# Optimization experiments

Hardware: AMD Instinct MI355X
Metric: run time of the kernel (lower is better)

Reference implementation:

```python
import jax, jax.numpy as jnp
import numpy as np

B, C, H, W = 4, 256, 64, 64
DQ = C // 8

def setup_inputs() -> dict:
    key = jax.random.key(0)
    ks = jax.random.split(key, 7)
    x = jax.random.normal(ks[0], (B, C, H, W), dtype=jnp.float32)
    # 1x1 convs == per-pixel linear layers: weight [out, in], bias [out]
    Wq = jax.random.normal(ks[1], (DQ, C), dtype=jnp.float32) * (1.0 / np.sqrt(C))
    bq = jax.random.normal(ks[2], (DQ,), dtype=jnp.float32) * 0.01
    Wk = jax.random.normal(ks[3], (DQ, C), dtype=jnp.float32) * (1.0 / np.sqrt(C))
    bk = jax.random.normal(ks[4], (DQ,), dtype=jnp.float32) * 0.01
    Wv = jax.random.normal(ks[5], (C, C), dtype=jnp.float32) * (1.0 / np.sqrt(C))
    bv = jax.random.normal(ks[6], (C,), dtype=jnp.float32) * 0.01
    return {"x": x, "Wq": Wq, "bq": bq, "Wk": Wk, "bk": bk, "Wv": Wv, "bv": bv}

def reference(x, Wq, bq, Wk, bk, Wv, bv):
    b, c, h, w = x.shape
    n = h * w
    xf = x.reshape(b, c, n)                                  # [b,c,n]
    Q = jnp.einsum('dc,bcn->bnd', Wq, xf) + bq               # [b,n,dq]
    K = jnp.einsum('dc,bcn->bdn', Wk, xf) + bk[None, :, None]  # [b,dq,n]
    A = jax.nn.softmax(jnp.einsum('bnd,bdm->bnm', Q, K), axis=-1)  # [b,n,n]
    V = jnp.einsum('oc,bcn->bon', Wv, xf) + bv[None, :, None]      # [b,c,n]
    # torch: bmm(V, A^T) -> out[b,c,i] = sum_j V[b,c,j] * A[b,i,j]
    out = jnp.einsum('bcj,bij->bci', V, A)
    return x + out.reshape(b, c, h, w)
```

## Files before the change

kernel.cpp:

```cpp
#include <hip/hip_runtime.h>
#include <math.h>

#define BB 4
#define CC 256
#define NN 4096
#define DQ 32
#define LOG2E 1.44269504f

typedef _Float16 half8 __attribute__((ext_vector_type(8)));
typedef _Float16 half4 __attribute__((ext_vector_type(4)));
typedef float float4v __attribute__((ext_vector_type(4)));

__global__ __launch_bounds__(64) void prep_kernel(
    const float* __restrict__ Wq, const float* __restrict__ bq,
    const float* __restrict__ Wk, const float* __restrict__ bk,
    const float* __restrict__ Wv, const float* __restrict__ bv,
    _Float16* __restrict__ Wh, float* __restrict__ bh)
{
    int o = blockIdx.x, t = threadIdx.x;
    const float* src; float scale = 1.0f, bias;
    if (o < DQ)            { src = Wq + o * CC;        scale = LOG2E; bias = bq[o] * LOG2E; }
    else if (o < 2 * DQ)   { src = Wk + (o - DQ) * CC;                bias = bk[o - DQ]; }
    else                   { src = Wv + (o - 2 * DQ) * CC;            bias = bv[o - 2 * DQ]; }
    float4 v = *(const float4*)(src + t * 4);
    half4 h = { (_Float16)(v.x * scale), (_Float16)(v.y * scale),
                (_Float16)(v.z * scale), (_Float16)(v.w * scale) };
    *(half4*)(Wh + o * CC + t * 4) = h;
    if (t == 0) bh[o] = bias;
}

__global__ __launch_bounds__(256) void proj_kernel(
    const float* __restrict__ x, const _Float16* __restrict__ Wh,
    const float* __restrict__ bh,
    _Float16* __restrict__ Qt, _Float16* __restrict__ Kt,
    _Float16* __restrict__ Vh)
{
    __shared__ _Float16 xl[32 * 256];
    __shared__ _Float16 os_qk[32 * 72];
    __shared__ _Float16 os_v[256 * 40];

    const int tid = threadIdx.x;
    const int lane = tid & 63, w = tid >> 6;
    const int i16 = lane & 15, q = lane >> 4;
    const int n0 = blockIdx.x * 32, b = blockIdx.y;

    const float* xb = x + (size_t)b * CC * NN + n0;
    #pragma unroll
    for (int u = 0; u < 8; ++u) {
        int idx = u * 256 + tid;
        int c = idx >> 3, n4 = idx & 7;
        float4 v = *(const float4*)(xb + (size_t)c * NN + n4 * 4);
        int chunk = c >> 3, cl = c & 7;
        float vv[4] = {v.x, v.y, v.z, v.w};
        #pragma unroll
        for (int e = 0; e < 4; ++e) {
            int n = n4 * 4 + e;
            xl[n * 256 + ((chunk ^ n) * 8) + cl] = (_Float16)vv[e];
        }
    }

    float4v acc[5][2];
    const int obase = 80 * w;
    #pragma unroll
    for (int ot = 0; ot < 5; ++ot) {
        float4 b4 = *(const float4*)(bh + obase + 16 * ot + 4 * q);
        #pragma unroll
        for (int nt = 0; nt < 2; ++nt)
            acc[ot][nt] = (float4v){b4.x, b4.y, b4.z, b4.w};
    }
    __syncthreads();

    #pragma unroll
    for (int k = 0; k < 8; ++k) {
        half8 af[5], bf[2];
        #pragma unroll
        for (int ot = 0; ot < 5; ++ot)
            af[ot] = *(const half8*)(Wh + (size_t)(obase + 16 * ot + i16) * CC + k * 32 + 8 * q);
        #pragma unroll
        for (int nt = 0; nt < 2; ++nt) {
            int n = 16 * nt + i16;
            bf[nt] = *(const half8*)&xl[n * 256 + (((4 * k + q) ^ n) * 8)];
        }
        #pragma unroll
        for (int ot = 0; ot < 5; ++ot)
            #pragma unroll
            for (int nt = 0; nt < 2; ++nt)
                acc[ot][nt] = __builtin_amdgcn_mfma_f32_16x16x32_f16(af[ot], bf[nt], acc[ot][nt], 0, 0, 0);
    }

    #pragma unroll
    for (int ot = 0; ot < 5; ++ot) {
        int og = obase + 16 * ot;
        #pragma unroll
        for (int nt = 0; nt < 2; ++nt) {
            int n = 16 * nt + i16;
            if (og < 64) {
                half4 hv = { (_Float16)acc[ot][nt][0], (_Float16)acc[ot][nt][1],
                             (_Float16)acc[ot][nt][2], (_Float16)acc[ot][nt][3] };
                *(half4*)&os_qk[n * 72 + og + 4 * q] = hv;
            } else {
                int cb = og - 64 + 4 * q;
                #pragma unroll
                for (int r = 0; r < 4; ++r)
                    os_v[(cb + r) * 40 + n] = (_Float16)acc[ot][nt][r];
            }
        }
    }
    __syncthreads();

    _Float16* Qtb = Qt + (size_t)b * NN * DQ;
    _Float16* Ktb = Kt + (size_t)b * NN * DQ;
    {
        int n = tid >> 3, p = tid & 7;
        half8 hv = *(const half8*)&os_qk[n * 72 + 8 * p];
        if (p < 4) *(half8*)(Qtb + (size_t)(n0 + n) * DQ + 8 * p) = hv;
        else       *(half8*)(Ktb + (size_t)(n0 + n) * DQ + 8 * (p - 4)) = hv;
    }
    _Float16* Vb = Vh + (size_t)b * CC * NN;
    #pragma unroll
    for (int u = 0; u < 4; ++u) {
        int c = u * 64 + (tid >> 2), p = tid & 3;
        half8 hv = *(const half8*)&os_v[c * 40 + 8 * p];
        *(half8*)(Vb + (size_t)c * NN + n0 + 8 * p) = hv;
    }
}

__global__ __launch_bounds__(256) void attn_kernel(
    const float* __restrict__ x,
    const _Float16* __restrict__ Qt, const _Float16* __restrict__ Kt,
    const _Float16* __restrict__ Vh,
    float* __restrict__ out)
{
    __shared__ _Float16 k2[2][16 * 64];
    __shared__ _Float16 v2[3][64 * 64];
    __shared__ _Float16 ps[2][32 * 40];
    __shared__ float    stx[4][32];

    const int tid = threadIdx.x;
    const int w = tid >> 6, lane = tid & 63;
    const int i16 = lane & 15, q = lane >> 4;
    const int i0 = blockIdx.x * 32, cs = blockIdx.y, b = blockIdx.z;
    const int c0 = cs * 128;

    const _Float16* Ktb = Kt + (size_t)b * NN * DQ;
    const _Float16* Vb  = Vh + (size_t)b * CC * NN + (size_t)c0 * NN;

    half8 qb[2];
    {
        const _Float16* Qtb = Qt + (size_t)b * NN * DQ;
        qb[0] = *(const half8*)(Qtb + (size_t)(i0 + i16) * DQ + 8 * q);
        qb[1] = *(const half8*)(Qtb + (size_t)(i0 + 16 + i16) * DQ + 8 * q);
    }

    float mA[2] = {-INFINITY, -INFINITY};
    {
        const _Float16* kq = Ktb + (size_t)(1024 * w) * DQ;
        half8 kf[4];
        #pragma unroll
        for (int u = 0; u < 4; ++u)
            kf[u] = *(const half8*)(kq + (size_t)(16 * u + i16) * DQ + 8 * q);
        for (int t = 0; t < 64; t += 4) {
            #pragma unroll
            for (int u = 0; u < 4; ++u) {
                half8 ka = kf[u];
                int nt = t + 4 + u;
                if (nt < 64)
                    kf[u] = *(const half8*)(kq + (size_t)(16 * nt + i16) * DQ + 8 * q);
                float4v z = {0.f, 0.f, 0.f, 0.f};
                float4v s0 = __builtin_amdgcn_mfma_f32_16x16x32_f16(ka, qb[0], z, 0, 0, 0);
                float4v s1 = __builtin_amdgcn_mfma_f32_16x16x32_f16(ka, qb[1], z, 0, 0, 0);
                mA[0] = fmaxf(mA[0], fmaxf(fmaxf(s0[0], s0[1]), fmaxf(s0[2], s0[3])));
                mA[1] = fmaxf(mA[1], fmaxf(fmaxf(s1[0], s1[1]), fmaxf(s1[2], s1[3])));
            }
        }
        #pragma unroll
        for (int it = 0; it < 2; ++it) {
            mA[it] = fmaxf(mA[it], __shfl_xor(mA[it], 16, 64));
            mA[it] = fmaxf(mA[it], __shfl_xor(mA[it], 32, 64));
        }
        if (q == 0) { stx[w][i16] = mA[0]; stx[w][16 + i16] = mA[1]; }
    }
    __syncthreads();

    float m2v[2];
    #pragma unroll
    for (int it = 0; it < 2; ++it) {
        int r = 16 * it + i16;
        m2v[it] = fmaxf(fmaxf(stx[0][r], stx[1][r]), fmaxf(stx[2][r], stx[3][r]));
    }

    float4v O[2][2];
    #pragma unroll
    for (int ct = 0; ct < 2; ++ct)
        #pragma unroll
        for (int it = 0; it < 2; ++it)
            O[ct][it] = (float4v){0.f, 0.f, 0.f, 0.f};
    float lB = 0.f;

    const int jK = (tid & 127) >> 2, dgK = tid & 3;
    const int kaddr = (jK >> 1) * 64 + (((dgK + 4 * (jK & 1)) ^ ((jK >> 1) & 7)) * 8);
    const int cV = tid >> 2, jgV = tid & 3;
    int vaddr[2];
    #pragma unroll
    for (int u = 0; u < 2; ++u) {
        int c = 64 * u + cV;
        vaddr[u] = (c >> 1) * 64 + (((jgV + 4 * (c & 1)) ^ ((c >> 1) & 7)) * 8);
    }
    const int jS = 16 * (w & 1) + i16;
    const int ka_off = (jS >> 1) * 64 + (((q + 4 * (jS & 1)) ^ ((jS >> 1) & 7)) * 8);
    const int ih = w >> 1;
    int va_off[2];
    #pragma unroll
    for (int ct = 0; ct < 2; ++ct) {
        int c = 32 * w + 16 * ct + i16;
        va_off[ct] = (c >> 1) * 64 + (((q + 4 * (c & 1)) ^ ((c >> 1) & 7)) * 8);
    }
    const int pswr = (16 * ih + i16) * 40 + 16 * (w & 1) + 4 * q;
    const int pb_off0 = i16 * 40 + 8 * q;
    const int pb_off1 = (16 + i16) * 40 + 8 * q;

    half8 kv, vv[2];
    if (w < 2) kv = *(const half8*)(Ktb + (size_t)jK * DQ + 8 * dgK);
    #pragma unroll
    for (int u = 0; u < 2; ++u)
        vv[u] = *(const half8*)(Vb + (size_t)(64 * u + cV) * NN + 8 * jgV);
    if (w < 2) *(half8*)&k2[0][kaddr] = kv;
    #pragma unroll
    for (int u = 0; u < 2; ++u)
        *(half8*)&v2[0][vaddr[u]] = vv[u];
    if (w < 2) kv = *(const half8*)(Ktb + (size_t)(32 + jK) * DQ + 8 * dgK);
    #pragma unroll
    for (int u = 0; u < 2; ++u)
        vv[u] = *(const half8*)(Vb + (size_t)(64 * u + cV) * NN + 32 + 8 * jgV);

    for (int t = 0; t <= 128; ++t) {
        __syncthreads();
        if (t < 127) {
            if (w < 2) *(half8*)&k2[(t + 1) & 1][kaddr] = kv;
            const int vn = (t + 1) % 3;
            #pragma unroll
            for (int u = 0; u < 2; ++u)
                *(half8*)&v2[vn][vaddr[u]] = vv[u];
        }
        if (t < 126) {
            int jn = (t + 2) * 32;
            if (w < 2) kv = *(const half8*)(Ktb + (size_t)(jn + jK) * DQ + 8 * dgK);
            #pragma unroll
            for (int u = 0; u < 2; ++u)
                vv[u] = *(const half8*)(Vb + (size_t)(64 * u + cV) * NN + jn + 8 * jgV);
        }
        if (t > 0) {
            const _Float16* psp = ps[(t - 1) & 1];
            const _Float16* vp  = v2[(t - 1) % 3];
            half8 pbv0 = *(const half8*)&psp[pb_off0];
            half8 pbv1 = *(const half8*)&psp[pb_off1];
            half8 va0  = *(const half8*)&vp[va_off[0]];
            half8 va1  = *(const half8*)&vp[va_off[1]];
            __builtin_amdgcn_s_setprio(1);
            O[0][0] = __builtin_amdgcn_mfma_f32_16x16x32_f16(va0, pbv0, O[0][0], 0, 0, 0);
            O[0][1] = __builtin_amdgcn_mfma_f32_16x16x32_f16(va0, pbv1, O[0][1], 0, 0, 0);
            O[1][0] = __builtin_amdgcn_mfma_f32_16x16x32_f16(va1, pbv0, O[1][0], 0, 0, 0);
            O[1][1] = __builtin_amdgcn_mfma_f32_16x16x32_f16(va1, pbv1, O[1][1], 0, 0, 0);
            __builtin_amdgcn_s_setprio(0);
        }
        if (t < 128) {
            half8 ka = *(const half8*)&k2[t & 1][ka_off];
            float4v z = {0.f, 0.f, 0.f, 0.f};
            float4v s = __builtin_amdgcn_mfma_f32_16x16x32_f16(ka, qb[ih], z, 0, 0, 0);
            float p0 = exp2f(s[0] - m2v[ih]);
            float p1 = exp2f(s[1] - m2v[ih]);
            float p2 = exp2f(s[2] - m2v[ih]);
            float p3 = exp2f(s[3] - m2v[ih]);
            lB += (p0 + p1) + (p2 + p3);
            half4 hv = { (_Float16)p0, (_Float16)p1, (_Float16)p2, (_Float16)p3 };
            *(half4*)&ps[t & 1][pswr] = hv;
        }
    }

    lB += __shfl_xor(lB, 16, 64);
    lB += __shfl_xor(lB, 32, 64);
    if (q == 0) stx[w][i16] = lB;
    __syncthreads();
    float linv[2];
    #pragma unroll
    for (int it = 0; it < 2; ++it)
        linv[it] = 1.0f / (stx[2 * it][i16] + stx[2 * it + 1][i16]);

    const float* xb = x + (size_t)b * CC * NN;
    float* ob = out + (size_t)b * CC * NN;
    #pragma unroll
    for (int ct = 0; ct < 2; ++ct)
        #pragma unroll
        for (int it = 0; it < 2; ++it)
            #pragma unroll
            for (int r = 0; r < 4; ++r) {
                int c = c0 + 32 * w + 16 * ct + 4 * q + r;
                size_t idx = (size_t)c * NN + i0 + 16 * it + i16;
                ob[idx] = xb[idx] + O[ct][it][r] * linv[it];
            }
}

extern "C" void kernel_launch(void* const* d_in, const int* in_sizes, int n_in,
                              void* d_out, int out_size, void* d_ws, size_t ws_size,
                              hipStream_t stream) {
    const float* x  = (const float*)d_in[0];
    const float* Wq = (const float*)d_in[1];
    const float* bq = (const float*)d_in[2];
    const float* Wk = (const float*)d_in[3];
    const float* bk = (const float*)d_in[4];
    const float* Wv = (const float*)d_in[5];
    const float* bv = (const float*)d_in[6];
    float* out = (float*)d_out;

    char* ws = (char*)d_ws;
    _Float16* Wh = (_Float16*)(ws);
    float*    bh = (float*)(ws + 163840);
    _Float16* Qt = (_Float16*)(ws + 262144);
    _Float16* Kt = (_Float16*)(ws + 1310720);
    _Float16* Vh = (_Float16*)(ws + 2359296);

    prep_kernel<<<dim3(320), 64, 0, stream>>>(Wq, bq, Wk, bk, Wv, bv, Wh, bh);
    proj_kernel<<<dim3(NN / 32, BB), 256, 0, stream>>>(x, Wh, bh, Qt, Kt, Vh);
    attn_kernel<<<dim3(NN / 32, 2, BB), 256, 0, stream>>>(x, Qt, Kt, Vh, out);
}
```

Measured before the change: 200.0 us.

## Cover all channels per block and load V straight into registers

The attention kernel now handles all 256 output channels in one block instead of splitting channels across two blocks. This removes the duplicated QK^T and softmax work, and the K tile grows to 64 keys per step. V fragments are loaded from global memory directly into registers, double-buffered across two iterations, so the shared-memory V staging and its triple buffer go away. The cost is half as many blocks (less parallelism on the GPU), more accumulator and V registers per thread, and uncoalesced-looking per-lane V loads.

```diff
diff --git a/kernel.cpp b/kernel.cpp
--- a/kernel.cpp
+++ b/kernel.cpp
@@ -131,19 +131,17 @@
     const _Float16* __restrict__ Vh,
     float* __restrict__ out)
 {
-    __shared__ _Float16 k2[2][16 * 64];
-    __shared__ _Float16 v2[3][64 * 64];
-    __shared__ _Float16 ps[2][32 * 40];
+    __shared__ _Float16 k2[2][64 * 32];
+    __shared__ _Float16 ps2[2][32 * 72];
     __shared__ float    stx[4][32];
 
     const int tid = threadIdx.x;
     const int w = tid >> 6, lane = tid & 63;
     const int i16 = lane & 15, q = lane >> 4;
-    const int i0 = blockIdx.x * 32, cs = blockIdx.y, b = blockIdx.z;
-    const int c0 = cs * 128;
+    const int i0 = blockIdx.x * 32, b = blockIdx.y;
 
     const _Float16* Ktb = Kt + (size_t)b * NN * DQ;
-    const _Float16* Vb  = Vh + (size_t)b * CC * NN + (size_t)c0 * NN;
+    const _Float16* Vb  = Vh + (size_t)b * CC * NN;
 
     half8 qb[2];
     {
@@ -189,112 +187,114 @@
         m2v[it] = fmaxf(fmaxf(stx[0][r], stx[1][r]), fmaxf(stx[2][r], stx[3][r]));
     }
 
-    float4v O[2][2];
-    #pragma unroll
-    for (int ct = 0; ct < 2; ++ct)
+    float4v O[4][2];
+    #pragma unroll
+    for (int ct = 0; ct < 4; ++ct)
         #pragma unroll
         for (int it = 0; it < 2; ++it)
             O[ct][it] = (float4v){0.f, 0.f, 0.f, 0.f};
-    float lB = 0.f;
-
-    const int jK = (tid & 127) >> 2, dgK = tid & 3;
-    const int kaddr = (jK >> 1) * 64 + (((dgK + 4 * (jK & 1)) ^ ((jK >> 1) & 7)) * 8);
-    const int cV = tid >> 2, jgV = tid & 3;
-    int vaddr[2];
-    #pragma unroll
-    for (int u = 0; u < 2; ++u) {
-        int c = 64 * u + cV;
-        vaddr[u] = (c >> 1) * 64 + (((jgV + 4 * (c & 1)) ^ ((c >> 1) & 7)) * 8);
-    }
-    const int jS = 16 * (w & 1) + i16;
-    const int ka_off = (jS >> 1) * 64 + (((q + 4 * (jS & 1)) ^ ((jS >> 1) & 7)) * 8);
-    const int ih = w >> 1;
-    int va_off[2];
-    #pragma unroll
-    for (int ct = 0; ct < 2; ++ct) {
-        int c = 32 * w + 16 * ct + i16;
-        va_off[ct] = (c >> 1) * 64 + (((q + 4 * (c & 1)) ^ ((c >> 1) & 7)) * 8);
-    }
-    const int pswr = (16 * ih + i16) * 40 + 16 * (w & 1) + 4 * q;
-    const int pb_off0 = i16 * 40 + 8 * q;
-    const int pb_off1 = (16 + i16) * 40 + 8 * q;
-
-    half8 kv, vv[2];
-    if (w < 2) kv = *(const half8*)(Ktb + (size_t)jK * DQ + 8 * dgK);
-    #pragma unroll
-    for (int u = 0; u < 2; ++u)
-        vv[u] = *(const half8*)(Vb + (size_t)(64 * u + cV) * NN + 8 * jgV);
-    if (w < 2) *(half8*)&k2[0][kaddr] = kv;
-    #pragma unroll
-    for (int u = 0; u < 2; ++u)
-        *(half8*)&v2[0][vaddr[u]] = vv[u];
-    if (w < 2) kv = *(const half8*)(Ktb + (size_t)(32 + jK) * DQ + 8 * dgK);
-    #pragma unroll
-    for (int u = 0; u < 2; ++u)
-        vv[u] = *(const half8*)(Vb + (size_t)(64 * u + cV) * NN + 32 + 8 * jgV);
-
-    for (int t = 0; t <= 128; ++t) {
+    float lB[2] = {0.f, 0.f};
+
+    const int jK = tid >> 2, dgK = tid & 3;
+    const int kaddr = jK * 32 + ((dgK ^ (jK & 3)) * 8);
+    const int jS = 16 * w + i16;
+    const int ka_off = jS * 32 + ((q ^ (jS & 3)) * 8);
+
+    const _Float16* vp[8];
+    #pragma unroll
+    for (int ct = 0; ct < 4; ++ct)
+        #pragma unroll
+        for (int ks = 0; ks < 2; ++ks)
+            vp[ct * 2 + ks] = Vb + (size_t)(64 * w + 16 * ct + i16) * NN + 32 * ks + 8 * q;
+
+    half8 kv;
+    kv = *(const half8*)(Ktb + (size_t)jK * DQ + 8 * dgK);
+    *(half8*)&k2[0][kaddr] = kv;
+    kv = *(const half8*)(Ktb + (size_t)(64 + jK) * DQ + 8 * dgK);
+
+    half8 vbA[8], vbB[8];
+
+    auto stageK = [&](int t) {
+        if (t < 63) *(half8*)&k2[(t + 1) & 1][kaddr] = kv;
+        if (t < 62) kv = *(const half8*)(Ktb + (size_t)((t + 2) * 64 + jK) * DQ + 8 * dgK);
+    };
+    auto loadV = [&](half8* dst, int t) {
+        #pragma unroll
+        for (int u = 0; u < 8; ++u)
+            dst[u] = *(const half8*)(vp[u] + 64 * t);
+    };
+    auto pvPhase = [&](const half8* va, const _Float16* psp) {
+        half8 pb[2][2];
+        #pragma unroll
+        for (int ks = 0; ks < 2; ++ks)
+            #pragma unroll
+            for (int it = 0; it < 2; ++it)
+                pb[ks][it] = *(const half8*)&psp[(16 * it + i16) * 72 + 32 * ks + 8 * q];
+        __builtin_amdgcn_s_setprio(1);
+        #pragma unroll
+        for (int ct = 0; ct < 4; ++ct)
+            #pragma unroll
+            for (int ks = 0; ks < 2; ++ks)
+                #pragma unroll
+                for (int it = 0; it < 2; ++it)
+                    O[ct][it] = __builtin_amdgcn_mfma_f32_16x16x32_f16(va[ct * 2 + ks], pb[ks][it], O[ct][it], 0, 0, 0);
+        __builtin_amdgcn_s_setprio(0);
+    };
+    auto sPhase = [&](int t) {
+        half8 ka = *(const half8*)&k2[t & 1][ka_off];
+        _Float16* psc = ps2[t & 1];
+        #pragma unroll
+        for (int it = 0; it < 2; ++it) {
+            float4v z = {0.f, 0.f, 0.f, 0.f};
+            float4v s = __builtin_amdgcn_mfma_f32_16x16x32_f16(ka, qb[it], z, 0, 0, 0);
+            float p0 = exp2f(s[0] - m2v[it]);
+            float p1 = exp2f(s[1] - m2v[it]);
+            float p2 = exp2f(s[2] - m2v[it]);
+            float p3 = exp2f(s[3] - m2v[it]);
+            lB[it] += (p0 + p1) + (p2 + p3);
+            half4 hv = { (_Float16)p0, (_Float16)p1, (_Float16)p2, (_Float16)p3 };
+            *(half4*)&psc[(16 * it + i16) * 72 + 16 * w + 4 * q] = hv;
+        }
+    };
+
+    for (int tt = 0; tt < 64; tt += 2) {
         __syncthreads();
-        if (t < 127) {
-            if (w < 2) *(half8*)&k2[(t + 1) & 1][kaddr] = kv;
-            const int vn = (t + 1) % 3;
-            #pragma unroll
-            for (int u = 0; u < 2; ++u)
-                *(half8*)&v2[vn][vaddr[u]] = vv[u];
-        }
-        if (t < 126) {
-            int jn = (t + 2) * 32;
-            if (w < 2) kv = *(const half8*)(Ktb + (size_t)(jn + jK) * DQ + 8 * dgK);
-            #pragma unroll
-            for (int u = 0; u < 2; ++u)
-                vv[u] = *(const half8*)(Vb + (size_t)(64 * u + cV) * NN + jn + 8 * jgV);
-        }
-        if (t > 0) {
-            const _Float16* psp = ps[(t - 1) & 1];
-            const _Float16* vp  = v2[(t - 1) % 3];
-            half8 pbv0 = *(const half8*)&psp[pb_off0];
-            half8 pbv1 = *(const half8*)&psp[pb_off1];
-            half8 va0  = *(const half8*)&vp[va_off[0]];
-            half8 va1  = *(const half8*)&vp[va_off[1]];
-            __builtin_amdgcn_s_setprio(1);
-            O[0][0] = __builtin_amdgcn_mfma_f32_16x16x32_f16(va0, pbv0, O[0][0], 0, 0, 0);
-            O[0][1] = __builtin_amdgcn_mfma_f32_16x16x32_f16(va0, pbv1, O[0][1], 0, 0, 0);
-            O[1][0] = __builtin_amdgcn_mfma_f32_16x16x32_f16(va1, pbv0, O[1][0], 0, 0, 0);
-            O[1][1] = __builtin_amdgcn_mfma_f32_16x16x32_f16(va1, pbv1, O[1][1], 0, 0, 0);
-            __builtin_amdgcn_s_setprio(0);
-        }
-        if (t < 128) {
-            half8 ka = *(const half8*)&k2[t & 1][ka_off];
-            float4v z = {0.f, 0.f, 0.f, 0.f};
-            float4v s = __builtin_amdgcn_mfma_f32_16x16x32_f16(ka, qb[ih], z, 0, 0, 0);
-            float p0 = exp2f(s[0] - m2v[ih]);
-            float p1 = exp2f(s[1] - m2v[ih]);
-            float p2 = exp2f(s[2] - m2v[ih]);
-            float p3 = exp2f(s[3] - m2v[ih]);
-            lB += (p0 + p1) + (p2 + p3);
-            half4 hv = { (_Float16)p0, (_Float16)p1, (_Float16)p2, (_Float16)p3 };
-            *(half4*)&ps[t & 1][pswr] = hv;
-        }
-    }
-
-    lB += __shfl_xor(lB, 16, 64);
-    lB += __shfl_xor(lB, 32, 64);
-    if (q == 0) stx[w][i16] = lB;
+        stageK(tt);
+        loadV(vbA, tt);
+        if (tt > 0) pvPhase(vbB, ps2[1]);
+        sPhase(tt);
+        __syncthreads();
+        stageK(tt + 1);
+        loadV(vbB, tt + 1);
+        pvPhase(vbA, ps2[0]);
+        sPhase(tt + 1);
+    }
+    __syncthreads();
+    pvPhase(vbB, ps2[1]);
+
+    #pragma unroll
+    for (int it = 0; it < 2; ++it) {
+        lB[it] += __shfl_xor(lB[it], 16, 64);
+        lB[it] += __shfl_xor(lB[it], 32, 64);
+    }
+    if (q == 0) { stx[w][i16] = lB[0]; stx[w][16 + i16] = lB[1]; }
     __syncthreads();
     float linv[2];
     #pragma unroll
-    for (int it = 0; it < 2; ++it)
-        linv[it] = 1.0f / (stx[2 * it][i16] + stx[2 * it + 1][i16]);
+    for (int it = 0; it < 2; ++it) {
+        int r = 16 * it + i16;
+        linv[it] = 1.0f / ((stx[0][r] + stx[1][r]) + (stx[2][r] + stx[3][r]));
+    }
 
     const float* xb = x + (size_t)b * CC * NN;
     float* ob = out + (size_t)b * CC * NN;
     #pragma unroll
-    for (int ct = 0; ct < 2; ++ct)
+    for (int ct = 0; ct < 4; ++ct)
         #pragma unroll
         for (int it = 0; it < 2; ++it)
             #pragma unroll
             for (int r = 0; r < 4; ++r) {
-                int c = c0 + 32 * w + 16 * ct + 4 * q + r;
+                int c = 64 * w + 16 * ct + 4 * q + r;
                 size_t idx = (size_t)c * NN + i0 + 16 * it + i16;
                 ob[idx] = xb[idx] + O[ct][it][r] * linv[it];
             }
@@ -321,5 +321,5 @@
 
     prep_kernel<<<dim3(320), 64, 0, stream>>>(Wq, bq, Wk, bk, Wv, bv, Wh, bh);
     proj_kernel<<<dim3(NN / 32, BB), 256, 0, stream>>>(x, Wh, bh, Qt, Kt, Vh);
-    attn_kernel<<<dim3(NN / 32, 2, BB), 256, 0, stream>>>(x, Qt, Kt, Vh, out);
+    attn_kernel<<<dim3(NN / 32, BB), 256, 0, stream>>>(x, Qt, Kt, Vh, out);
 }
```

Result: slower. 216.3 us (+8.2%).
